# Performance work log

Hardware: AMD Instinct MI355X
Metric: run time of the kernel (lower is better)

## Reference

```python
import jax, jax.numpy as jnp
import numpy as np

ALPHA = 0.2  # LeakyReLU negative slope
NEG_INF = -9e15  # matches torch -9000000000000000.0


def setup_inputs() -> dict:
    key = jax.random.key(0)
    k1, k2, k3, k4, k5, k6 = jax.random.split(key, 6)
    N, F_in, F_out = 4096, 512, 256
    adj = jax.random.randint(k1, (N, N), 0, 2, dtype=jnp.int32)
    h = jax.random.normal(k2, (N, F_in), dtype=jnp.float32)
    # proj: Linear(F_in, F_out)
    W = jax.random.normal(k3, (F_in, F_out), dtype=jnp.float32) * (1.0 / np.sqrt(F_in))
    b = jax.random.normal(k4, (F_out,), dtype=jnp.float32) * 0.01
    # proj_a: Linear(2*F_out, 1) split into the two halves acting on src/dst features
    a1 = jax.random.normal(k5, (F_out,), dtype=jnp.float32) * (1.0 / np.sqrt(2 * F_out))
    a2 = jax.random.normal(k6, (F_out,), dtype=jnp.float32) * (1.0 / np.sqrt(2 * F_out))
    a_b = jnp.zeros((), dtype=jnp.float32)
    return {"adj": adj, "h": h, "W": W, "b": b, "a1": a1, "a2": a2, "a_b": a_b}


def reference(adj, h, W, b, a1, a2, a_b):
    # wh = proj(h): [N, F_out]
    wh = h @ W + b
    # Fused form of the N x N x 2F concat + Linear(2F,1):
    # logits[i, j] = wh[i] . a1 + wh[j] . a2 + a_b
    f_src = wh @ a1  # [N]
    f_dst = wh @ a2  # [N]
    e = jax.nn.leaky_relu(f_src[:, None] + f_dst[None, :] + a_b, negative_slope=ALPHA)
    e = jnp.where(adj > 0, e, NEG_INF)
    att = jax.nn.softmax(e, axis=-1)  # F.softmax legacy dim=1 for 2D
    # dropout: inference mode (no-op) for deterministic reference
    out = att @ wh  # [N, F_out]
    return jax.nn.elu(out)  # concat=True
```

## Files before the change

kernel.cpp:

```cpp
#include <hip/hip_runtime.h>

#define NN   4096
#define FIN  512
#define FOUT 256
#define ALPHA 0.2f

typedef __attribute__((ext_vector_type(8))) short short8;
typedef __attribute__((ext_vector_type(4))) float f32x4;
typedef unsigned short u16;

__device__ __forceinline__ u16 f2bf(float x) {
    union { float f; unsigned u; } v; v.f = x;
    unsigned r = v.u + 0x7FFF + ((v.u >> 16) & 1);
    return (u16)(r >> 16);
}

__global__ __launch_bounds__(256) void k_wt(const float* __restrict__ W,
                                            u16* __restrict__ Wt) {
    __shared__ float s[64 * 65];
    const int t  = threadIdx.x;
    const int f0 = blockIdx.x * 64;
    const int k0 = blockIdx.y * 64;
    #pragma unroll
    for (int p = 0; p < 4; ++p) {
        int q = t + 256 * p, rr = q >> 4, cc = q & 15;
        float4 w4 = *(const float4*)&W[(size_t)(k0 + rr) * FOUT + f0 + cc * 4];
        s[(cc * 4 + 0) * 65 + rr] = w4.x;
        s[(cc * 4 + 1) * 65 + rr] = w4.y;
        s[(cc * 4 + 2) * 65 + rr] = w4.z;
        s[(cc * 4 + 3) * 65 + rr] = w4.w;
    }
    __syncthreads();
    #pragma unroll
    for (int p = 0; p < 4; ++p) {
        int q = t + 256 * p, f = q >> 4, kg = q & 15;
        ushort4 o;
        o.x = f2bf(s[f * 65 + kg * 4 + 0]);
        o.y = f2bf(s[f * 65 + kg * 4 + 1]);
        o.z = f2bf(s[f * 65 + kg * 4 + 2]);
        o.w = f2bf(s[f * 65 + kg * 4 + 3]);
        *(ushort4*)&Wt[(size_t)(f0 + f) * FIN + k0 + kg * 4] = o;
    }
}

#define HS 520
__global__ __launch_bounds__(256) void k_proj(const float* __restrict__ h,
                                              const u16* __restrict__ Wt,
                                              const float* __restrict__ bias,
                                              const float* __restrict__ a1,
                                              const float* __restrict__ a2,
                                              u16* __restrict__ whT,
                                              float* __restrict__ psrc,
                                              float* __restrict__ pdst) {
    __shared__ u16   s_h[32 * HS];
    __shared__ float s_red[4 * 32];
    const int t  = threadIdx.x;
    const int f0 = blockIdx.x * 64;
    const int i0 = blockIdx.y * 32;
    #pragma unroll
    for (int p = 0; p < 16; ++p) {
        int q = t + 256 * p, row = q >> 7, c4 = q & 127;
        float4 v = *(const float4*)&h[(size_t)(i0 + row) * FIN + c4 * 4];
        ushort4 o; o.x = f2bf(v.x); o.y = f2bf(v.y); o.z = f2bf(v.z); o.w = f2bf(v.w);
        *(ushort4*)&s_h[row * HS + c4 * 4] = o;
    }
    __syncthreads();
    const int w = t >> 6, l = t & 63, n = l & 15, quad = l >> 4;
    const int hh = w & 1, fh = w >> 1;
    f32x4 acc[2] = {{0.f,0.f,0.f,0.f},{0.f,0.f,0.f,0.f}};
    #pragma unroll
    for (int k0 = 0; k0 < FIN; k0 += 32) {
        short8 a  = *(const short8*)&s_h[(hh * 16 + n) * HS + k0 + quad * 8];
        short8 b0 = *(const short8*)&Wt[(size_t)(f0 + fh * 32 + n) * FIN + k0 + quad * 8];
        short8 b1 = *(const short8*)&Wt[(size_t)(f0 + fh * 32 + 16 + n) * FIN + k0 + quad * 8];
        acc[0] = __builtin_amdgcn_mfma_f32_16x16x32_bf16(a, b0, acc[0], 0, 0, 0);
        acc[1] = __builtin_amdgcn_mfma_f32_16x16x32_bf16(a, b1, acc[1], 0, 0, 0);
    }
    u16* wt_tile = whT + (size_t)(i0 >> 5) * (FOUT * 32);
    float a1v[2], a2v[2];
    a1v[0] = a1[f0 + fh * 32 + n];      a1v[1] = a1[f0 + fh * 32 + 16 + n];
    a2v[0] = a2[f0 + fh * 32 + n];      a2v[1] = a2[f0 + fh * 32 + 16 + n];
    float ps[4] = {0.f,0.f,0.f,0.f}, pd[4] = {0.f,0.f,0.f,0.f};
    #pragma unroll
    for (int u = 0; u < 2; ++u) {
        const int f = f0 + fh * 32 + u * 16 + n;
        const float bv = bias[f];
        #pragma unroll
        for (int r = 0; r < 4; ++r) {
            float val = acc[u][r] + bv;
            wt_tile[f * 32 + hh * 16 + quad * 4 + r] = f2bf(val);
            ps[r] += val * a1v[u];
            pd[r] += val * a2v[u];
        }
    }
    #pragma unroll
    for (int m = 1; m < 16; m <<= 1) {
        #pragma unroll
        for (int r = 0; r < 4; ++r) { ps[r] += __shfl_xor(ps[r], m); pd[r] += __shfl_xor(pd[r], m); }
    }
    if (n == 0) {
        #pragma unroll
        for (int r = 0; r < 4; ++r) {
            int il = hh * 16 + quad * 4 + r;
            s_red[fh * 32 + il]       = ps[r];
            s_red[64 + fh * 32 + il]  = pd[r];
        }
    }
    __syncthreads();
    if (t < 32) {
        psrc[(size_t)blockIdx.x * NN + i0 + t] = s_red[t]      + s_red[32 + t];
        pdst[(size_t)blockIdx.x * NN + i0 + t] = s_red[64 + t] + s_red[96 + t];
    }
}

#define BI 32
#define TJ 64
#define PS 72
#define CC 8
#define JCHUNK (NN / CC)
#define NITER  (JCHUNK / TJ)
__global__ __launch_bounds__(256) void k_attn(const int* __restrict__ adj,
                                              const u16* __restrict__ whT,
                                              const float* __restrict__ psrc,
                                              const float* __restrict__ pdst,
                                              const float* __restrict__ ab,
                                              float* __restrict__ part,
                                              float* __restrict__ psum) {
    __shared__ u16   s_p[2][BI * PS];
    __shared__ float s_fd[JCHUNK];
    __shared__ float s_fs[BI];
    const int t  = threadIdx.x;
    const int i0 = blockIdx.x * BI;
    const int c  = blockIdx.y;
    const int jbeg = c * JCHUNK;
    const int jq = t & 15, rh = t >> 4;
    const int w = t >> 6, l = t & 63, n = l & 15, quad = l >> 4;

    if (t < BI) {
        s_fs[t] = psrc[i0 + t] + psrc[NN + i0 + t] + psrc[2 * NN + i0 + t]
                + psrc[3 * NN + i0 + t] + ab[0];
    }
    if (t < JCHUNK / 4) {
        float4 v0 = ((const float4*)&pdst[jbeg])[t];
        float4 v1 = ((const float4*)&pdst[NN + jbeg])[t];
        float4 v2 = ((const float4*)&pdst[2 * NN + jbeg])[t];
        float4 v3 = ((const float4*)&pdst[3 * NN + jbeg])[t];
        float4 o;
        o.x = v0.x + v1.x + v2.x + v3.x; o.y = v0.y + v1.y + v2.y + v3.y;
        o.z = v0.z + v1.z + v2.z + v3.z; o.w = v0.w + v1.w + v2.w + v3.w;
        ((float4*)s_fd)[t] = o;
    }
    __syncthreads();
    const float fs0 = s_fs[rh], fs1 = s_fs[rh + 16];

    f32x4 acc[2][4] = {{{0.f,0.f,0.f,0.f},{0.f,0.f,0.f,0.f},{0.f,0.f,0.f,0.f},{0.f,0.f,0.f,0.f}},
                       {{0.f,0.f,0.f,0.f},{0.f,0.f,0.f,0.f},{0.f,0.f,0.f,0.f},{0.f,0.f,0.f,0.f}}};
    float rs0 = 0.f, rs1 = 0.f;
    int4 av0 = *(const int4*)&adj[(size_t)(i0 + rh) * NN + jbeg + jq * 4];
    int4 av1 = *(const int4*)&adj[(size_t)(i0 + rh + 16) * NN + jbeg + jq * 4];

    for (int it = 0; it < NITER; ++it) {
        const int j0 = jbeg + it * TJ;
        u16* sp = s_p[it & 1];
        float4 fdv = *(const float4*)&s_fd[it * TJ + jq * 4];
        ushort4 o0, o1;
        {
            float x, p;
            x = fs0 + fdv.x; x = x > 0.f ? x : ALPHA * x; p = av0.x > 0 ? __expf(x) : 0.f; o0.x = f2bf(p); rs0 += p;
            x = fs0 + fdv.y; x = x > 0.f ? x : ALPHA * x; p = av0.y > 0 ? __expf(x) : 0.f; o0.y = f2bf(p); rs0 += p;
            x = fs0 + fdv.z; x = x > 0.f ? x : ALPHA * x; p = av0.z > 0 ? __expf(x) : 0.f; o0.z = f2bf(p); rs0 += p;
            x = fs0 + fdv.w; x = x > 0.f ? x : ALPHA * x; p = av0.w > 0 ? __expf(x) : 0.f; o0.w = f2bf(p); rs0 += p;
            x = fs1 + fdv.x; x = x > 0.f ? x : ALPHA * x; p = av1.x > 0 ? __expf(x) : 0.f; o1.x = f2bf(p); rs1 += p;
            x = fs1 + fdv.y; x = x > 0.f ? x : ALPHA * x; p = av1.y > 0 ? __expf(x) : 0.f; o1.y = f2bf(p); rs1 += p;
            x = fs1 + fdv.z; x = x > 0.f ? x : ALPHA * x; p = av1.z > 0 ? __expf(x) : 0.f; o1.z = f2bf(p); rs1 += p;
            x = fs1 + fdv.w; x = x > 0.f ? x : ALPHA * x; p = av1.w > 0 ? __expf(x) : 0.f; o1.w = f2bf(p); rs1 += p;
        }
        *(ushort4*)&sp[rh * PS + jq * 4]        = o0;
        *(ushort4*)&sp[(rh + 16) * PS + jq * 4] = o1;
        __syncthreads();
        if (it + 1 < NITER) {
            av0 = *(const int4*)&adj[(size_t)(i0 + rh) * NN + j0 + TJ + jq * 4];
            av1 = *(const int4*)&adj[(size_t)(i0 + rh + 16) * NN + j0 + TJ + jq * 4];
        }
        short8 b[2][4];
        #pragma unroll
        for (int s = 0; s < 2; ++s) {
            const u16* tb = whT + (size_t)((j0 >> 5) + s) * (FOUT * 32) + quad * 8;
            #pragma unroll
            for (int u = 0; u < 4; ++u)
                b[s][u] = *(const short8*)&tb[(w * 64 + u * 16 + n) * 32];
        }
        #pragma unroll
        for (int s = 0; s < 2; ++s) {
            short8 a0  = *(const short8*)&sp[n * PS + s * 32 + quad * 8];
            short8 a1f = *(const short8*)&sp[(16 + n) * PS + s * 32 + quad * 8];
            #pragma unroll
            for (int u = 0; u < 4; ++u) {
                acc[0][u] = __builtin_amdgcn_mfma_f32_16x16x32_bf16(a0,  b[s][u], acc[0][u], 0, 0, 0);
                acc[1][u] = __builtin_amdgcn_mfma_f32_16x16x32_bf16(a1f, b[s][u], acc[1][u], 0, 0, 0);
            }
        }
    }
    #pragma unroll
    for (int m = 8; m > 0; m >>= 1) {
        rs0 += __shfl_xor(rs0, m);
        rs1 += __shfl_xor(rs1, m);
    }
    if (jq == 0) {
        psum[(size_t)c * NN + i0 + rh]      = rs0;
        psum[(size_t)c * NN + i0 + rh + 16] = rs1;
    }
    float* pc = part + ((size_t)c * NN + i0) * FOUT;
    #pragma unroll
    for (int hf = 0; hf < 2; ++hf)
        #pragma unroll
        for (int u = 0; u < 4; ++u)
            #pragma unroll
            for (int r = 0; r < 4; ++r)
                pc[(size_t)(hf * 16 + quad * 4 + r) * FOUT + w * 64 + u * 16 + n] = acc[hf][u][r];
}

__global__ __launch_bounds__(256) void k_fin(const float* __restrict__ part,
                                             const float* __restrict__ psum,
                                             float* __restrict__ out) {
    const int g = blockIdx.x * 256 + threadIdx.x;
    const int i = g >> 6;
    const size_t s4 = (size_t)NN * (FOUT / 4);
    float4 a = ((const float4*)part)[g];
    float s = psum[i];
    #pragma unroll
    for (int c = 1; c < CC; ++c) {
        float4 bb = ((const float4*)part)[g + (size_t)c * s4];
        a.x += bb.x; a.y += bb.y; a.z += bb.z; a.w += bb.w;
        s += psum[(size_t)c * NN + i];
    }
    const float inv = 1.0f / s;
    a.x *= inv; a.y *= inv; a.z *= inv; a.w *= inv;
    a.x = a.x > 0.f ? a.x : __expf(a.x) - 1.f;
    a.y = a.y > 0.f ? a.y : __expf(a.y) - 1.f;
    a.z = a.z > 0.f ? a.z : __expf(a.z) - 1.f;
    a.w = a.w > 0.f ? a.w : __expf(a.w) - 1.f;
    ((float4*)out)[g] = a;
}

extern "C" void kernel_launch(void* const* d_in, const int* in_sizes, int n_in,
                              void* d_out, int out_size, void* d_ws, size_t ws_size,
                              hipStream_t stream) {
    const int*   adj = (const int*)  d_in[0];
    const float* h   = (const float*)d_in[1];
    const float* W   = (const float*)d_in[2];
    const float* b   = (const float*)d_in[3];
    const float* a1  = (const float*)d_in[4];
    const float* a2  = (const float*)d_in[5];
    const float* ab  = (const float*)d_in[6];
    float* out = (float*)d_out;

    float* psrc = (float*)d_ws;
    float* pdst = psrc + 4 * (size_t)NN;
    float* psum = pdst + 4 * (size_t)NN;
    float* part = psum + (size_t)CC * NN;
    u16*   Wt   = (u16*)(part + (size_t)CC * NN * FOUT);
    u16*   whT  = Wt + (size_t)FOUT * FIN;

    k_wt  <<<dim3(FOUT / 64, FIN / 64), 256, 0, stream>>>(W, Wt);
    k_proj<<<dim3(FOUT / 64, NN / 32), 256, 0, stream>>>(h, Wt, b, a1, a2, whT, psrc, pdst);
    k_attn<<<dim3(NN / BI, CC), 256, 0, stream>>>(adj, whT, psrc, pdst, ab, part, psum);
    k_fin <<<(NN * FOUT / 4) / 256, 256, 0, stream>>>(part, psum, out);
}
```

Baseline: 165.6 us.

## Compute attention probabilities directly in MFMA A-fragment registers, drop LDS staging

New measurement: 184.1 us. 1.11x slower.

```diff
diff --git a/kernel.cpp b/kernel.cpp
--- a/kernel.cpp
+++ b/kernel.cpp
@@ -113,10 +113,9 @@
     }
 }
 
-#define BI 32
-#define TJ 64
-#define PS 72
-#define CC 8
+#define BI 16
+#define TJ 32
+#define CC 4
 #define JCHUNK (NN / CC)
 #define NITER  (JCHUNK / TJ)
 __global__ __launch_bounds__(256) void k_attn(const int* __restrict__ adj,
@@ -126,21 +125,14 @@
                                               const float* __restrict__ ab,
                                               float* __restrict__ part,
                                               float* __restrict__ psum) {
-    __shared__ u16   s_p[2][BI * PS];
     __shared__ float s_fd[JCHUNK];
-    __shared__ float s_fs[BI];
     const int t  = threadIdx.x;
     const int i0 = blockIdx.x * BI;
     const int c  = blockIdx.y;
     const int jbeg = c * JCHUNK;
-    const int jq = t & 15, rh = t >> 4;
     const int w = t >> 6, l = t & 63, n = l & 15, quad = l >> 4;
 
-    if (t < BI) {
-        s_fs[t] = psrc[i0 + t] + psrc[NN + i0 + t] + psrc[2 * NN + i0 + t]
-                + psrc[3 * NN + i0 + t] + ab[0];
-    }
-    if (t < JCHUNK / 4) {
+    {
         float4 v0 = ((const float4*)&pdst[jbeg])[t];
         float4 v1 = ((const float4*)&pdst[NN + jbeg])[t];
         float4 v2 = ((const float4*)&pdst[2 * NN + jbeg])[t];
@@ -150,74 +142,54 @@
         o.z = v0.z + v1.z + v2.z + v3.z; o.w = v0.w + v1.w + v2.w + v3.w;
         ((float4*)s_fd)[t] = o;
     }
-    __syncthreads();
-    const float fs0 = s_fs[rh], fs1 = s_fs[rh + 16];
-
-    f32x4 acc[2][4] = {{{0.f,0.f,0.f,0.f},{0.f,0.f,0.f,0.f},{0.f,0.f,0.f,0.f},{0.f,0.f,0.f,0.f}},
-                       {{0.f,0.f,0.f,0.f},{0.f,0.f,0.f,0.f},{0.f,0.f,0.f,0.f},{0.f,0.f,0.f,0.f}}};
-    float rs0 = 0.f, rs1 = 0.f;
-    int4 av0 = *(const int4*)&adj[(size_t)(i0 + rh) * NN + jbeg + jq * 4];
-    int4 av1 = *(const int4*)&adj[(size_t)(i0 + rh + 16) * NN + jbeg + jq * 4];
+    const float fsm = psrc[i0 + n] + psrc[NN + i0 + n] + psrc[2 * NN + i0 + n]
+                    + psrc[3 * NN + i0 + n] + ab[0];
+    __syncthreads();
+
+    const int* arow = adj + (size_t)(i0 + n) * NN + jbeg + quad * 8;
+    int4 a0 = *(const int4*)arow;
+    int4 a1 = *(const int4*)(arow + 4);
+
+    f32x4 acc[4] = {{0.f,0.f,0.f,0.f},{0.f,0.f,0.f,0.f},{0.f,0.f,0.f,0.f},{0.f,0.f,0.f,0.f}};
+    float rs = 0.f;
 
     for (int it = 0; it < NITER; ++it) {
-        const int j0 = jbeg + it * TJ;
-        u16* sp = s_p[it & 1];
-        float4 fdv = *(const float4*)&s_fd[it * TJ + jq * 4];
-        ushort4 o0, o1;
+        const int jo = it * TJ;
+        float4 g0 = *(const float4*)&s_fd[jo + quad * 8];
+        float4 g1 = *(const float4*)&s_fd[jo + quad * 8 + 4];
+        short8 af;
         {
             float x, p;
-            x = fs0 + fdv.x; x = x > 0.f ? x : ALPHA * x; p = av0.x > 0 ? __expf(x) : 0.f; o0.x = f2bf(p); rs0 += p;
-            x = fs0 + fdv.y; x = x > 0.f ? x : ALPHA * x; p = av0.y > 0 ? __expf(x) : 0.f; o0.y = f2bf(p); rs0 += p;
-            x = fs0 + fdv.z; x = x > 0.f ? x : ALPHA * x; p = av0.z > 0 ? __expf(x) : 0.f; o0.z = f2bf(p); rs0 += p;
-            x = fs0 + fdv.w; x = x > 0.f ? x : ALPHA * x; p = av0.w > 0 ? __expf(x) : 0.f; o0.w = f2bf(p); rs0 += p;
-            x = fs1 + fdv.x; x = x > 0.f ? x : ALPHA * x; p = av1.x > 0 ? __expf(x) : 0.f; o1.x = f2bf(p); rs1 += p;
-            x = fs1 + fdv.y; x = x > 0.f ? x : ALPHA * x; p = av1.y > 0 ? __expf(x) : 0.f; o1.y = f2bf(p); rs1 += p;
-            x = fs1 + fdv.z; x = x > 0.f ? x : ALPHA * x; p = av1.z > 0 ? __expf(x) : 0.f; o1.z = f2bf(p); rs1 += p;
-            x = fs1 + fdv.w; x = x > 0.f ? x : ALPHA * x; p = av1.w > 0 ? __expf(x) : 0.f; o1.w = f2bf(p); rs1 += p;
-        }
-        *(ushort4*)&sp[rh * PS + jq * 4]        = o0;
-        *(ushort4*)&sp[(rh + 16) * PS + jq * 4] = o1;
-        __syncthreads();
+            x = fsm + g0.x; x = x > 0.f ? x : ALPHA * x; p = a0.x > 0 ? __expf(x) : 0.f; af[0] = (short)f2bf(p); rs += p;
+            x = fsm + g0.y; x = x > 0.f ? x : ALPHA * x; p = a0.y > 0 ? __expf(x) : 0.f; af[1] = (short)f2bf(p); rs += p;
+            x = fsm + g0.z; x = x > 0.f ? x : ALPHA * x; p = a0.z > 0 ? __expf(x) : 0.f; af[2] = (short)f2bf(p); rs += p;
+            x = fsm + g0.w; x = x > 0.f ? x : ALPHA * x; p = a0.w > 0 ? __expf(x) : 0.f; af[3] = (short)f2bf(p); rs += p;
+            x = fsm + g1.x; x = x > 0.f ? x : ALPHA * x; p = a1.x > 0 ? __expf(x) : 0.f; af[4] = (short)f2bf(p); rs += p;
+            x = fsm + g1.y; x = x > 0.f ? x : ALPHA * x; p = a1.y > 0 ? __expf(x) : 0.f; af[5] = (short)f2bf(p); rs += p;
+            x = fsm + g1.z; x = x > 0.f ? x : ALPHA * x; p = a1.z > 0 ? __expf(x) : 0.f; af[6] = (short)f2bf(p); rs += p;
+            x = fsm + g1.w; x = x > 0.f ? x : ALPHA * x; p = a1.w > 0 ? __expf(x) : 0.f; af[7] = (short)f2bf(p); rs += p;
+        }
         if (it + 1 < NITER) {
-            av0 = *(const int4*)&adj[(size_t)(i0 + rh) * NN + j0 + TJ + jq * 4];
-            av1 = *(const int4*)&adj[(size_t)(i0 + rh + 16) * NN + j0 + TJ + jq * 4];
-        }
-        short8 b[2][4];
-        #pragma unroll
-        for (int s = 0; s < 2; ++s) {
-            const u16* tb = whT + (size_t)((j0 >> 5) + s) * (FOUT * 32) + quad * 8;
-            #pragma unroll
-            for (int u = 0; u < 4; ++u)
-                b[s][u] = *(const short8*)&tb[(w * 64 + u * 16 + n) * 32];
-        }
-        #pragma unroll
-        for (int s = 0; s < 2; ++s) {
-            short8 a0  = *(const short8*)&sp[n * PS + s * 32 + quad * 8];
-            short8 a1f = *(const short8*)&sp[(16 + n) * PS + s * 32 + quad * 8];
-            #pragma unroll
-            for (int u = 0; u < 4; ++u) {
-                acc[0][u] = __builtin_amdgcn_mfma_f32_16x16x32_bf16(a0,  b[s][u], acc[0][u], 0, 0, 0);
-                acc[1][u] = __builtin_amdgcn_mfma_f32_16x16x32_bf16(a1f, b[s][u], acc[1][u], 0, 0, 0);
-            }
-        }
-    }
-    #pragma unroll
-    for (int m = 8; m > 0; m >>= 1) {
-        rs0 += __shfl_xor(rs0, m);
-        rs1 += __shfl_xor(rs1, m);
-    }
-    if (jq == 0) {
-        psum[(size_t)c * NN + i0 + rh]      = rs0;
-        psum[(size_t)c * NN + i0 + rh + 16] = rs1;
-    }
-    float* pc = part + ((size_t)c * NN + i0) * FOUT;
-    #pragma unroll
-    for (int hf = 0; hf < 2; ++hf)
-        #pragma unroll
-        for (int u = 0; u < 4; ++u)
-            #pragma unroll
-            for (int r = 0; r < 4; ++r)
-                pc[(size_t)(hf * 16 + quad * 4 + r) * FOUT + w * 64 + u * 16 + n] = acc[hf][u][r];
+            a0 = *(const int4*)(arow + TJ);
+            a1 = *(const int4*)(arow + TJ + 4);
+            arow += TJ;
+        }
+        const u16* tb = whT + (size_t)((jbeg + jo) >> 5) * (FOUT * 32) + quad * 8;
+        #pragma unroll
+        for (int u = 0; u < 4; ++u) {
+            short8 b = *(const short8*)&tb[(w * 64 + u * 16 + n) * 32];
+            acc[u] = __builtin_amdgcn_mfma_f32_16x16x32_bf16(af, b, acc[u], 0, 0, 0);
+        }
+    }
+    rs += __shfl_xor(rs, 16);
+    rs += __shfl_xor(rs, 32);
+    if (t < BI) psum[(size_t)c * NN + i0 + t] = rs;
+    float* pc = part + ((size_t)c * NN + i0) * FOUT + w * 64;
+    #pragma unroll
+    for (int u = 0; u < 4; ++u)
+        #pragma unroll
+        for (int r = 0; r < 4; ++r)
+            pc[(size_t)(quad * 4 + r) * FOUT + u * 16 + n] = acc[u][r];
 }
 
 __global__ __launch_bounds__(256) void k_fin(const float* __restrict__ part,
```
